# Optimization experiments

Measured on AMD Instinct MI355X. Metric: run time of the kernel, lower is better.

Reference implementation:

```python
import jax, jax.numpy as jnp
import numpy as np

EPS = 1e-5

def conv2d(x, w, b):
    # x: [B,C,H,W], w: [O,I,kh,kw], VALID padding, stride 1
    y = jax.lax.conv_general_dilated(x, w, (1, 1), 'VALID',
                                     dimension_numbers=('NCHW', 'OIHW', 'NCHW'))
    return y + b[None, :, None, None]

def batchnorm(x, g, b):
    # training-mode BN: batch statistics over (N,H,W), biased variance (torch semantics)
    m = jnp.mean(x, axis=(0, 2, 3), keepdims=True)
    v = jnp.mean((x - m) ** 2, axis=(0, 2, 3), keepdims=True)
    return g[None, :, None, None] * (x - m) / jnp.sqrt(v + EPS) + b[None, :, None, None]

def maxpool2(x):
    return jax.lax.reduce_window(x, -jnp.inf, jax.lax.max,
                                 (1, 1, 2, 2), (1, 1, 2, 2), 'VALID')

def self_attention(x, qw, qb, kw, kb, vw, vb, gamma):
    # x: [B,C,H,W]; qw/kw: [C//8, C]; vw: [C, C] (1x1 convs)
    B, C, H, W = x.shape
    xf = x.reshape(B, C, H * W)                               # [B,C,N]
    q = jnp.einsum('oc,bcn->bon', qw, xf) + qb[None, :, None]  # [B,C//8,N]
    k = jnp.einsum('oc,bcn->bon', kw, xf) + kb[None, :, None]
    v = jnp.einsum('oc,bcn->bon', vw, xf) + vb[None, :, None]  # [B,C,N]
    energy = jnp.einsum('bcn,bcm->bnm', q, k)                  # [B,N,N] (query n, key m)
    attn = jax.nn.softmax(energy, axis=-1)
    out = jnp.einsum('bcm,bnm->bcn', v, attn)                  # [B,C,N]
    return gamma * out.reshape(B, C, H, W) + x

def setup_inputs() -> dict:
    key = jax.random.key(0)
    ks = jax.random.split(key, 20)
    s = 0.05
    d = {}
    d['x'] = jax.random.normal(ks[0], (1, 3, 256, 256), jnp.float32)
    d['conv1_w'] = jax.random.normal(ks[1], (32, 3, 3, 3), jnp.float32) * s
    d['conv1_b'] = jnp.zeros((32,), jnp.float32)
    d['bn1_g'] = jnp.ones((32,), jnp.float32)
    d['bn1_b'] = jnp.zeros((32,), jnp.float32)
    d['a1_qw'] = jax.random.normal(ks[2], (4, 32), jnp.float32) * s
    d['a1_qb'] = jnp.zeros((4,), jnp.float32)
    d['a1_kw'] = jax.random.normal(ks[3], (4, 32), jnp.float32) * s
    d['a1_kb'] = jnp.zeros((4,), jnp.float32)
    d['a1_vw'] = jax.random.normal(ks[4], (32, 32), jnp.float32) * s
    d['a1_vb'] = jnp.zeros((32,), jnp.float32)
    d['a1_gamma'] = jnp.ones((1,), jnp.float32)
    d['conv2_w'] = jax.random.normal(ks[5], (64, 32, 3, 3), jnp.float32) * s
    d['conv2_b'] = jnp.zeros((64,), jnp.float32)
    d['bn2_g'] = jnp.ones((64,), jnp.float32)
    d['bn2_b'] = jnp.zeros((64,), jnp.float32)
    d['a2_qw'] = jax.random.normal(ks[6], (8, 64), jnp.float32) * s
    d['a2_qb'] = jnp.zeros((8,), jnp.float32)
    d['a2_kw'] = jax.random.normal(ks[7], (8, 64), jnp.float32) * s
    d['a2_kb'] = jnp.zeros((8,), jnp.float32)
    d['a2_vw'] = jax.random.normal(ks[8], (64, 64), jnp.float32) * s
    d['a2_vb'] = jnp.zeros((64,), jnp.float32)
    d['a2_gamma'] = jnp.ones((1,), jnp.float32)
    d['fc_w'] = jax.random.normal(ks[9], (50, 64 * 62 * 62), jnp.float32) * 0.002
    d['fc_b'] = jnp.zeros((50,), jnp.float32)
    return d

def reference(x, conv1_w, conv1_b, bn1_g, bn1_b,
              a1_qw, a1_qb, a1_kw, a1_kb, a1_vw, a1_vb, a1_gamma,
              conv2_w, conv2_b, bn2_g, bn2_b,
              a2_qw, a2_qb, a2_kw, a2_kb, a2_vw, a2_vb, a2_gamma,
              fc_w, fc_b):
    h = conv2d(x, conv1_w, conv1_b)                 # [B,32,254,254]
    h = jax.nn.relu(batchnorm(h, bn1_g, bn1_b))
    h = maxpool2(h)                                 # [B,32,127,127]
    h = self_attention(h, a1_qw, a1_qb, a1_kw, a1_kb, a1_vw, a1_vb, a1_gamma)
    h = conv2d(h, conv2_w, conv2_b)                 # [B,64,125,125]
    h = jax.nn.relu(batchnorm(h, bn2_g, bn2_b))
    h = maxpool2(h)                                 # [B,64,62,62]
    h = self_attention(h, a2_qw, a2_qb, a2_kw, a2_kb, a2_vw, a2_vb, a2_gamma)
    h = h.reshape(h.shape[0], -1)                   # [B, 64*62*62]
    return h @ fc_w.T + fc_b
```

## Files before the change

### kernel.cpp

```cpp
#include <hip/hip_runtime.h>
#include <hip/hip_bf16.h>

typedef float f32x4 __attribute__((ext_vector_type(4)));
typedef short bf16x8 __attribute__((ext_vector_type(8)));

__device__ inline unsigned short f2bf(float x) {
    __hip_bfloat16 h = __float2bfloat16(x);
    return *reinterpret_cast<unsigned short*>(&h);
}

template <int CIN, int ICB>
__launch_bounds__(256)
__global__ void conv3x3_rt_kernel(const float* __restrict__ src, int H, int W,
                                  const float* __restrict__ w,
                                  const float* __restrict__ b,
                                  float* __restrict__ dst, int OH, int OW,
                                  float* __restrict__ bn_accum) {
    __shared__ __align__(16) float xs[ICB][18][68];
    __shared__ __align__(16) float wsm[ICB][12];
    __shared__ float red[512];

    const int oc  = blockIdx.z;
    const int ox0 = blockIdx.x * 64;
    const int oy0 = blockIdx.y * 16;
    const int tid = threadIdx.x;
    const int ty  = tid >> 4;
    const int tx  = (tid & 15) << 2;

    float o0, o1, o2, o3;
    o0 = o1 = o2 = o3 = b[oc];

    const int scol   = tid & 63;
    const int sslot0 = tid >> 6;
    const bool colok = (ox0 + scol) < W;

    for (int icb = 0; icb < CIN; icb += ICB) {
        __syncthreads();
        {
            int s  = sslot0;
            int rr = sslot0;
            const float* gp = src + ((size_t)icb * H + oy0 + rr) * W + ox0 + scol;
            float* lp = &xs[0][0][0] + (size_t)s * 68 + scol;
            while (s < ICB * 18) {
                int y = oy0 + rr;
                *lp = (y < H && colok) ? *gp : 0.f;
                s += 4; rr += 4;
                gp += 4 * (size_t)W;
                lp += 4 * 68;
                if (rr >= 18) { rr -= 18; gp += ((size_t)H - 18) * W; }
            }
        }
        if (tid < ICB * 18) {
            int c = tid / 18, r = tid - c * 18;
            int y = oy0 + r;
            const float* gp = src + ((size_t)(icb + c) * H + y) * W + ox0 + 64;
            bool yok = (y < H);
            xs[c][r][64] = (yok && (ox0 + 64) < W) ? gp[0] : 0.f;
            xs[c][r][65] = (yok && (ox0 + 65) < W) ? gp[1] : 0.f;
        }
        if (tid < ICB * 9) {
            int c = tid / 9, j = tid - c * 9;
            wsm[c][j] = w[((size_t)oc * CIN + icb + c) * 9 + j];
        }
        __syncthreads();

        #pragma unroll
        for (int c = 0; c < ICB; ++c) {
            float wv[9];
            #pragma unroll
            for (int j = 0; j < 9; ++j) wv[j] = wsm[c][j];
            #pragma unroll
            for (int kh = 0; kh < 3; ++kh) {
                const float* xp = &xs[c][ty + kh][tx];
                f32x4 x03 = *(const f32x4*)xp;
                float x4 = xp[4], x5 = xp[5];
                const float w0 = wv[kh * 3], w1 = wv[kh * 3 + 1], w2 = wv[kh * 3 + 2];
                o0 = fmaf(x03[0], w0, o0); o0 = fmaf(x03[1], w1, o0); o0 = fmaf(x03[2], w2, o0);
                o1 = fmaf(x03[1], w0, o1); o1 = fmaf(x03[2], w1, o1); o1 = fmaf(x03[3], w2, o1);
                o2 = fmaf(x03[2], w0, o2); o2 = fmaf(x03[3], w1, o2); o2 = fmaf(x4,     w2, o2);
                o3 = fmaf(x03[3], w0, o3); o3 = fmaf(x4,     w1, o3); o3 = fmaf(x5,     w2, o3);
            }
        }
    }

    const int oy = oy0 + ty;
    const int ox = ox0 + tx;
    float s1 = 0.f, s2 = 0.f;
    if (oy < OH) {
        float* dp = dst + ((size_t)oc * OH + oy) * OW + ox;
        if (ox + 0 < OW) { dp[0] = o0; s1 += o0; s2 = fmaf(o0, o0, s2); }
        if (ox + 1 < OW) { dp[1] = o1; s1 += o1; s2 = fmaf(o1, o1, s2); }
        if (ox + 2 < OW) { dp[2] = o2; s1 += o2; s2 = fmaf(o2, o2, s2); }
        if (ox + 3 < OW) { dp[3] = o3; s1 += o3; s2 = fmaf(o3, o3, s2); }
    }
    red[tid]       = s1;
    red[256 + tid] = s2;
    __syncthreads();
    for (int off2 = 128; off2 > 0; off2 >>= 1) {
        if (tid < off2) {
            red[tid]       += red[tid + off2];
            red[256 + tid] += red[256 + tid + off2];
        }
        __syncthreads();
    }
    if (tid == 0) {
        atomicAdd(&bn_accum[oc * 2],     red[0]);
        atomicAdd(&bn_accum[oc * 2 + 1], red[256]);
    }
}

__global__ void bn_final_kernel(const float* __restrict__ sums, int C, int spatial,
                                const float* __restrict__ g, const float* __restrict__ bb,
                                float* __restrict__ inv_shift) {
    int c = threadIdx.x;
    if (c >= C) return;
    float m   = sums[c * 2] / (float)spatial;
    float var = sums[c * 2 + 1] / (float)spatial - m * m;
    float inv = g[c] * rsqrtf(var + 1e-5f);
    inv_shift[c * 2]     = inv;
    inv_shift[c * 2 + 1] = bb[c] - m * inv;
}

__global__ void bn_pool_kernel(const float* __restrict__ src,
                               const float* __restrict__ inv_shift,
                               int H, int W, int OH, int OW, int C,
                               float* __restrict__ dst) {
    int i = blockIdx.x * blockDim.x + threadIdx.x;
    if (i >= C * OH * OW) return;
    int ox = i % OW;
    int oy = (i / OW) % OH;
    int c  = i / (OW * OH);
    float inv = inv_shift[c * 2], sh = inv_shift[c * 2 + 1];
    const float* p = src + ((size_t)c * H + 2 * oy) * W + 2 * ox;
    float a = fmaxf(fmaf(p[0],     inv, sh), 0.f);
    float b = fmaxf(fmaf(p[1],     inv, sh), 0.f);
    float d = fmaxf(fmaf(p[W],     inv, sh), 0.f);
    float e = fmaxf(fmaf(p[W + 1], inv, sh), 0.f);
    dst[i] = fmaxf(fmaxf(a, b), fmaxf(d, e));
}

__global__ void qkv_proj_kernel(const float* __restrict__ xf, int N, int NP, int C, int Cqk,
                                const float* __restrict__ qw, const float* __restrict__ qb,
                                const float* __restrict__ kw, const float* __restrict__ kb,
                                const float* __restrict__ vw, const float* __restrict__ vb,
                                float* __restrict__ q, float* __restrict__ k,
                                unsigned short* __restrict__ v) {
    constexpr int OCG = 8;
    __shared__ float wl[OCG * 64 + OCG];
    const int g0 = blockIdx.y * OCG;
    const int tid = threadIdx.x;
    for (int i = tid; i < OCG * C; i += blockDim.x) {
        int o = i / C, cc = i % C;
        int oc = g0 + o;
        const float* wsrc = (oc < Cqk) ? (qw + oc * C)
                          : (oc < 2 * Cqk) ? (kw + (oc - Cqk) * C)
                          : (vw + (oc - 2 * Cqk) * C);
        wl[o * C + cc] = wsrc[cc];
    }
    if (tid < OCG) {
        int oc = g0 + tid;
        wl[OCG * C + tid] = (oc < Cqk) ? qb[oc]
                          : (oc < 2 * Cqk) ? kb[oc - Cqk]
                          : vb[oc - 2 * Cqk];
    }
    __syncthreads();
    int n = blockIdx.x * blockDim.x + tid;
    if (n >= N) return;
    float acc[OCG];
    #pragma unroll
    for (int o = 0; o < OCG; ++o) acc[o] = wl[OCG * C + o];
    for (int c = 0; c < C; ++c) {
        float xv = xf[(size_t)c * N + n];
        #pragma unroll
        for (int o = 0; o < OCG; ++o) acc[o] = fmaf(xv, wl[o * C + c], acc[o]);
    }
    #pragma unroll
    for (int o = 0; o < OCG; ++o) {
        int oc = g0 + o;
        if (oc < Cqk)            q[(size_t)oc * NP + n] = acc[o];
        else if (oc < 2 * Cqk)   k[(size_t)(oc - Cqk) * NP + n] = acc[o];
        else                     v[(size_t)(oc - 2 * Cqk) * NP + n] = f2bf(acc[o]);
    }
}

template <int CQK, int CV>
__launch_bounds__(256)
__global__ void flash_mfma_kernel(const float* __restrict__ q,
                                  const float* __restrict__ k,
                                  const unsigned short* __restrict__ v,
                                  int N, int NP, int chunk,
                                  float* __restrict__ l_part,
                                  float* __restrict__ acc_part) {
    constexpr int VS = 72;
    __shared__ float ksm[CQK * 64];
    __shared__ unsigned short vsm[CV * VS];
    const int tid  = threadIdx.x;
    const int wave = tid >> 6;
    const int lane = tid & 63;
    const int row  = lane & 15;
    const int g    = lane >> 4;
    const int s    = blockIdx.y;
    const int m0   = s * chunk;
    const int m1   = min(N, m0 + chunk);
    const int qb   = blockIdx.x * 64 + wave * 16;
    const int n    = qb + row;

    float qr[CQK];
    #pragma unroll
    for (int c = 0; c < CQK; ++c)
        qr[c] = (n < N) ? q[(size_t)c * NP + n] * 1.44269504f : 0.f;

    const int kc  = tid / 64,  kkk = tid % 64;
    const int vch = tid / 8,   vkk = (tid % 8) * 8;

    f32x4 acc[CV / 16];
    #pragma unroll
    for (int f = 0; f < CV / 16; ++f) acc[f] = (f32x4){0.f, 0.f, 0.f, 0.f};
    float lsum = 0.f;

    const int nchunks = (m1 - m0 + 63) >> 6;
    for (int t = 0; t < nchunks; ++t) {
        const int mt = m0 + t * 64;
        __syncthreads();
        #pragma unroll
        for (int cc = 0; cc < CQK / 4; ++cc)
            ksm[cc * 256 + tid] = k[(size_t)(kc + cc * 4) * NP + mt + kkk];
        #pragma unroll
        for (int vv = 0; vv < CV / 32; ++vv) {
            int ch = vch + vv * 32;
            ushort4 a0 = *(const ushort4*)&v[(size_t)ch * NP + mt + vkk];
            ushort4 a1 = *(const ushort4*)&v[(size_t)ch * NP + mt + vkk + 4];
            *(ushort4*)&vsm[ch * VS + vkk]     = a0;
            *(ushort4*)&vsm[ch * VS + vkk + 4] = a1;
        }
        __syncthreads();

        const bool tail = (mt + 64 > m1);
        #pragma unroll
        for (int h = 0; h < 2; ++h) {
            const int kk0 = h * 32 + 8 * g;
            f32x4 e0 = (f32x4){0.f, 0.f, 0.f, 0.f};
            f32x4 e1 = (f32x4){0.f, 0.f, 0.f, 0.f};
            #pragma unroll
            for (int c = 0; c < CQK; ++c) {
                f32x4 ka  = *(const f32x4*)&ksm[c * 64 + kk0];
                f32x4 kc2 = *(const f32x4*)&ksm[c * 64 + kk0 + 4];
                e0 += qr[c] * ka;
                e1 += qr[c] * kc2;
            }
            bf16x8 pfrag;
            if (!tail) {
                #pragma unroll
                for (int j = 0; j < 4; ++j) {
                    float p = exp2f(e0[j]); lsum += p; pfrag[j] = (short)f2bf(p);
                }
                #pragma unroll
                for (int j = 0; j < 4; ++j) {
                    float p = exp2f(e1[j]); lsum += p; pfrag[4 + j] = (short)f2bf(p);
                }
            } else {
                #pragma unroll
                for (int j = 0; j < 4; ++j) {
                    float p = (mt + kk0 + j < m1) ? exp2f(e0[j]) : 0.f;
                    lsum += p; pfrag[j] = (short)f2bf(p);
                }
                #pragma unroll
                for (int j = 0; j < 4; ++j) {
                    float p = (mt + kk0 + 4 + j < m1) ? exp2f(e1[j]) : 0.f;
                    lsum += p; pfrag[4 + j] = (short)f2bf(p);
                }
            }
            #pragma unroll
            for (int f = 0; f < CV / 16; ++f) {
                bf16x8 vf = *(const bf16x8*)&vsm[(f * 16 + row) * VS + kk0];
                acc[f] = __builtin_amdgcn_mfma_f32_16x16x32_bf16(pfrag, vf, acc[f], 0, 0, 0);
            }
        }
    }

    lsum += __shfl_xor(lsum, 16, 64);
    lsum += __shfl_xor(lsum, 32, 64);
    if (g == 0 && n < N) l_part[(size_t)s * N + n] = lsum;

    #pragma unroll
    for (int f = 0; f < CV / 16; ++f) {
        #pragma unroll
        for (int r2 = 0; r2 < 4; ++r2) {
            int nq = qb + 4 * g + r2;
            if (nq < N)
                acc_part[((size_t)s * N + nq) * CV + f * 16 + row] = acc[f][r2];
        }
    }
}

__global__ void combine_kernel(const float* __restrict__ acc_part,
                               const float* __restrict__ l_part,
                               int nsplit, int N, int CV,
                               const float* __restrict__ gamma,
                               const float* __restrict__ x_res,
                               float* __restrict__ out) {
    int n = blockIdx.x * blockDim.x + threadIdx.x;
    if (n >= N) return;
    int cv0 = blockIdx.y * 16;
    float l = 0.f;
    for (int s = 0; s < nsplit; ++s) l += l_part[(size_t)s * N + n];
    f32x4 a[4];
    #pragma unroll
    for (int t = 0; t < 4; ++t) a[t] = (f32x4){0.f, 0.f, 0.f, 0.f};
    for (int s = 0; s < nsplit; ++s) {
        const float* p = acc_part + ((size_t)s * N + n) * CV + cv0;
        #pragma unroll
        for (int t = 0; t < 4; ++t) a[t] += *(const f32x4*)(p + 4 * t);
    }
    float gs = gamma[0] / l;
    #pragma unroll
    for (int t = 0; t < 4; ++t)
        #pragma unroll
        for (int u = 0; u < 4; ++u) {
            int cv = cv0 + 4 * t + u;
            out[(size_t)cv * N + n] = fmaf(gs, a[t][u], x_res[(size_t)cv * N + n]);
        }
}

__global__ void fc_partial_kernel(const float* __restrict__ h, const float* __restrict__ w,
                                  int K, int nchunk, float* __restrict__ partial) {
    const int r = blockIdx.y, cb = blockIdx.x;
    const int chunk = K / nchunk;
    const int j0 = cb * chunk;
    const int j1 = (cb == nchunk - 1) ? K : j0 + chunk;
    const float* wr = w + (size_t)r * K;
    float s = 0.f;
    for (int j = j0 + (int)threadIdx.x * 4; j + 3 < j1; j += blockDim.x * 4) {
        float4 hv = *reinterpret_cast<const float4*>(h + j);
        float4 wv = *reinterpret_cast<const float4*>(wr + j);
        s += hv.x * wv.x + hv.y * wv.y + hv.z * wv.z + hv.w * wv.w;
    }
    __shared__ float red[256];
    red[threadIdx.x] = s;
    __syncthreads();
    for (int off = 128; off > 0; off >>= 1) {
        if ((int)threadIdx.x < off) red[threadIdx.x] += red[threadIdx.x + off];
        __syncthreads();
    }
    if (threadIdx.x == 0) partial[r * gridDim.x + cb] = red[0];
}

__global__ void fc_final_kernel(const float* __restrict__ partial,
                                const float* __restrict__ b, int nchunk,
                                float* __restrict__ out) {
    int r = threadIdx.x;
    if (r < 50) {
        float s = b[r];
        for (int i = 0; i < nchunk; ++i) s += partial[r * nchunk + i];
        out[r] = s;
    }
}

extern "C" void kernel_launch(void* const* d_in, const int* in_sizes, int n_in,
                              void* d_out, int out_size, void* d_ws, size_t ws_size,
                              hipStream_t stream) {
    const float* x    = (const float*)d_in[0];
    const float* c1w  = (const float*)d_in[1];
    const float* c1b  = (const float*)d_in[2];
    const float* bn1g = (const float*)d_in[3];
    const float* bn1b = (const float*)d_in[4];
    const float* a1qw = (const float*)d_in[5];
    const float* a1qb = (const float*)d_in[6];
    const float* a1kw = (const float*)d_in[7];
    const float* a1kb = (const float*)d_in[8];
    const float* a1vw = (const float*)d_in[9];
    const float* a1vb = (const float*)d_in[10];
    const float* a1g  = (const float*)d_in[11];
    const float* c2w  = (const float*)d_in[12];
    const float* c2b  = (const float*)d_in[13];
    const float* bn2g = (const float*)d_in[14];
    const float* bn2b = (const float*)d_in[15];
    const float* a2qw = (const float*)d_in[16];
    const float* a2qb = (const float*)d_in[17];
    const float* a2kw = (const float*)d_in[18];
    const float* a2kb = (const float*)d_in[19];
    const float* a2vw = (const float*)d_in[20];
    const float* a2vb = (const float*)d_in[21];
    const float* a2g  = (const float*)d_in[22];
    const float* fcw  = (const float*)d_in[23];
    const float* fcb  = (const float*)d_in[24];
    float* out = (float*)d_out;

    const int N1 = 127 * 127;
    const int N2 = 62 * 62;
    const int NP1 = (N1 + 63) & ~63;
    const int NP2 = (N2 + 63) & ~63;
    const int NS1 = 8, NS2 = 16;
    const int CH1 = 2048;
    const int CH2 = 256;

    char* base = (char*)d_ws;
    size_t off = 0;
    auto alloc = [&](size_t bytes) {
        void* p = base + off;
        off += (bytes + 63) & ~(size_t)63;
        return p;
    };
    float* h1     = (float*)alloc(sizeof(float) * 32 * 254 * 254);
    float* bnSums = (float*)alloc(sizeof(float) * 256);
    float* bnA    = (float*)alloc(sizeof(float) * 64);
    float* p1     = (float*)alloc(sizeof(float) * 32 * N1);
    float* q1     = (float*)alloc(sizeof(float) * 4 * NP1);
    float* k1     = (float*)alloc(sizeof(float) * 4 * NP1);
    unsigned short* v1 = (unsigned short*)alloc(sizeof(short) * 32 * NP1);
    float* l1     = (float*)alloc(sizeof(float) * NS1 * N1);
    float* a1p    = (float*)alloc(sizeof(float) * (size_t)NS1 * N1 * 32);
    float* ao1    = (float*)alloc(sizeof(float) * 32 * N1);
    float* h2     = (float*)alloc(sizeof(float) * 64 * 125 * 125);
    float* bnB    = (float*)alloc(sizeof(float) * 128);
    float* p2     = (float*)alloc(sizeof(float) * 64 * N2);
    float* q2     = (float*)alloc(sizeof(float) * 8 * NP2);
    float* k2     = (float*)alloc(sizeof(float) * 8 * NP2);
    unsigned short* v2 = (unsigned short*)alloc(sizeof(short) * 64 * NP2);
    float* l2     = (float*)alloc(sizeof(float) * NS2 * N2);
    float* a2p    = (float*)alloc(sizeof(float) * (size_t)NS2 * N2 * 64);
    float* ao2    = (float*)alloc(sizeof(float) * 64 * N2);
    float* fcp    = (float*)alloc(sizeof(float) * 2048);

    hipMemsetAsync(bnSums, 0, 256 * sizeof(float), stream);

    conv3x3_rt_kernel<3, 3><<<dim3(4, 16, 32), 256, 0, stream>>>(
        x, 256, 256, c1w, c1b, h1, 254, 254, bnSums);
    bn_final_kernel<<<1, 32, 0, stream>>>(bnSums, 32, 254 * 254, bn1g, bn1b, bnA);
    bn_pool_kernel<<<(32 * N1 + 255) / 256, 256, 0, stream>>>(
        h1, bnA, 254, 254, 127, 127, 32, p1);

    qkv_proj_kernel<<<dim3((N1 + 255) / 256, 5), 256, 0, stream>>>(
        p1, N1, NP1, 32, 4, a1qw, a1qb, a1kw, a1kb, a1vw, a1vb, q1, k1, v1);
    flash_mfma_kernel<4, 32><<<dim3((N1 + 63) / 64, NS1), 256, 0, stream>>>(
        q1, k1, v1, N1, NP1, CH1, l1, a1p);
    combine_kernel<<<dim3((N1 + 255) / 256, 2), 256, 0, stream>>>(
        a1p, l1, NS1, N1, 32, a1g, p1, ao1);

    conv3x3_rt_kernel<32, 8><<<dim3(2, 8, 64), 256, 0, stream>>>(
        ao1, 127, 127, c2w, c2b, h2, 125, 125, bnSums + 64);
    bn_final_kernel<<<1, 64, 0, stream>>>(bnSums + 64, 64, 125 * 125, bn2g, bn2b, bnB);
    bn_pool_kernel<<<(64 * N2 + 255) / 256, 256, 0, stream>>>(
        h2, bnB, 125, 125, 62, 62, 64, p2);

    qkv_proj_kernel<<<dim3((N2 + 255) / 256, 10), 256, 0, stream>>>(
        p2, N2, NP2, 64, 8, a2qw, a2qb, a2kw, a2kb, a2vw, a2vb, q2, k2, v2);
    flash_mfma_kernel<8, 64><<<dim3((N2 + 63) / 64, NS2), 256, 0, stream>>>(
        q2, k2, v2, N2, NP2, CH2, l2, a2p);
    combine_kernel<<<dim3((N2 + 255) / 256, 4), 256, 0, stream>>>(
        a2p, l2, NS2, N2, 64, a2g, p2, ao2);

    fc_partial_kernel<<<dim3(32, 50), 256, 0, stream>>>(ao2, fcw, 64 * N2, 32, fcp);
    fc_final_kernel<<<1, 64, 0, stream>>>(fcp, fcb, 32, out);
}
```

Baseline: 311.0 us.

## Compute QK energies with bf16 MFMA and double-buffer V tiles in flash attention

The projection kernel now writes Q (pre-scaled by log2e) and K as bf16 in a position-major layout. The flash kernel computes QK^T with 16x16x16 bf16 MFMA instead of scalar FMAs from shared K, and packs probabilities with v_cvt_pk_bf16. V tiles are prefetched into registers and double-buffered in LDS, so only one barrier is needed per tile. The first attention layer moves from 8 to 4 key splits with computed chunk sizes. Rounding Q and K to bf16 lowers the precision of the energies.

```diff
diff --git a/kernel.cpp b/kernel.cpp
--- a/kernel.cpp
+++ b/kernel.cpp
@@ -2,11 +2,19 @@
 #include <hip/hip_bf16.h>
 
 typedef float f32x4 __attribute__((ext_vector_type(4)));
-typedef short bf16x8 __attribute__((ext_vector_type(8)));
+typedef short bf16x4 __attribute__((ext_vector_type(4)));
+typedef unsigned short u16x4 __attribute__((ext_vector_type(4)));
+typedef unsigned short u16x8 __attribute__((ext_vector_type(8)));
 
 __device__ inline unsigned short f2bf(float x) {
     __hip_bfloat16 h = __float2bfloat16(x);
     return *reinterpret_cast<unsigned short*>(&h);
+}
+
+__device__ inline int cvt_pk_bf16(float a, float b) {
+    int r;
+    asm("v_cvt_pk_bf16_f32 %0, %1, %2" : "=v"(r) : "v"(a), "v"(b));
+    return r;
 }
 
 template <int CIN, int ICB>
@@ -143,8 +151,9 @@
                                 const float* __restrict__ qw, const float* __restrict__ qb,
                                 const float* __restrict__ kw, const float* __restrict__ kb,
                                 const float* __restrict__ vw, const float* __restrict__ vb,
-                                float* __restrict__ q, float* __restrict__ k,
-                                unsigned short* __restrict__ v) {
+                                unsigned short* __restrict__ qo,
+                                unsigned short* __restrict__ ko,
+                                unsigned short* __restrict__ vo) {
     constexpr int OCG = 8;
     __shared__ float wl[OCG * 64 + OCG];
     const int g0 = blockIdx.y * OCG;
@@ -174,108 +183,143 @@
         #pragma unroll
         for (int o = 0; o < OCG; ++o) acc[o] = fmaf(xv, wl[o * C + c], acc[o]);
     }
-    #pragma unroll
-    for (int o = 0; o < OCG; ++o) {
-        int oc = g0 + o;
-        if (oc < Cqk)            q[(size_t)oc * NP + n] = acc[o];
-        else if (oc < 2 * Cqk)   k[(size_t)(oc - Cqk) * NP + n] = acc[o];
-        else                     v[(size_t)(oc - 2 * Cqk) * NP + n] = f2bf(acc[o]);
+    const float LOG2E = 1.44269504f;
+    if (g0 < 2 * Cqk) {
+        if (Cqk == 4) {
+            u16x4 qs, ks;
+            #pragma unroll
+            for (int j = 0; j < 4; ++j) {
+                qs[j] = f2bf(acc[j] * LOG2E);
+                ks[j] = f2bf(acc[4 + j]);
+            }
+            *(u16x4*)&qo[(size_t)n * 4] = qs;
+            *(u16x4*)&ko[(size_t)n * 4] = ks;
+        } else {
+            unsigned short* dst = (g0 == 0) ? qo : ko;
+            float sc = (g0 == 0) ? LOG2E : 1.f;
+            u16x4 a, bb2;
+            #pragma unroll
+            for (int j = 0; j < 4; ++j) {
+                a[j]   = f2bf(acc[j] * sc);
+                bb2[j] = f2bf(acc[4 + j] * sc);
+            }
+            *(u16x4*)&dst[(size_t)n * 8]     = a;
+            *(u16x4*)&dst[(size_t)n * 8 + 4] = bb2;
+        }
+    } else {
+        #pragma unroll
+        for (int o = 0; o < OCG; ++o)
+            vo[(size_t)(g0 + o - 2 * Cqk) * NP + n] = f2bf(acc[o]);
     }
 }
 
 template <int CQK, int CV>
 __launch_bounds__(256)
-__global__ void flash_mfma_kernel(const float* __restrict__ q,
-                                  const float* __restrict__ k,
+__global__ void flash_mfma_kernel(const unsigned short* __restrict__ qbf,
+                                  const unsigned short* __restrict__ kbf,
                                   const unsigned short* __restrict__ v,
                                   int N, int NP, int chunk,
                                   float* __restrict__ l_part,
                                   float* __restrict__ acc_part) {
     constexpr int VS = 72;
-    __shared__ float ksm[CQK * 64];
-    __shared__ unsigned short vsm[CV * VS];
+    __shared__ unsigned short vsm[2][CV * VS];
     const int tid  = threadIdx.x;
     const int wave = tid >> 6;
     const int lane = tid & 63;
-    const int row  = lane & 15;
+    const int lq   = lane & 15;
     const int g    = lane >> 4;
     const int s    = blockIdx.y;
     const int m0   = s * chunk;
     const int m1   = min(N, m0 + chunk);
     const int qb   = blockIdx.x * 64 + wave * 16;
-    const int n    = qb + row;
-
-    float qr[CQK];
-    #pragma unroll
-    for (int c = 0; c < CQK; ++c)
-        qr[c] = (n < N) ? q[(size_t)c * NP + n] * 1.44269504f : 0.f;
-
-    const int kc  = tid / 64,  kkk = tid % 64;
-    const int vch = tid / 8,   vkk = (tid % 8) * 8;
+    const int n    = qb + lq;
+
+    bf16x4 qf = (bf16x4){0, 0, 0, 0};
+    if (g * 4 < CQK)
+        qf = *(const bf16x4*)&qbf[(size_t)n * CQK + 4 * g];
+
+    const int vch = tid >> 3;
+    const int vkk = (tid & 7) * 8;
 
     f32x4 acc[CV / 16];
     #pragma unroll
     for (int f = 0; f < CV / 16; ++f) acc[f] = (f32x4){0.f, 0.f, 0.f, 0.f};
     float lsum = 0.f;
 
-    const int nchunks = (m1 - m0 + 63) >> 6;
-    for (int t = 0; t < nchunks; ++t) {
-        const int mt = m0 + t * 64;
+    const int nch = (m1 - m0 + 63) >> 6;
+
+    u16x8 vreg[CV / 32];
+    #pragma unroll
+    for (int vv = 0; vv < CV / 32; ++vv)
+        vreg[vv] = *(const u16x8*)&v[(size_t)(vch + 32 * vv) * NP + m0 + vkk];
+    #pragma unroll
+    for (int vv = 0; vv < CV / 32; ++vv)
+        *(u16x8*)&vsm[0][(vch + 32 * vv) * VS + vkk] = vreg[vv];
+    __syncthreads();
+
+    for (int t = 0; t < nch; ++t) {
+        const int mt  = m0 + t * 64;
+        const int cur = t & 1;
+        const int mtn = (t + 1 < nch) ? mt + 64 : mt;
+        #pragma unroll
+        for (int vv = 0; vv < CV / 32; ++vv)
+            vreg[vv] = *(const u16x8*)&v[(size_t)(vch + 32 * vv) * NP + mtn + vkk];
+
+        bf16x4 kf[4];
+        #pragma unroll
+        for (int tt = 0; tt < 4; ++tt) {
+            kf[tt] = (bf16x4){0, 0, 0, 0};
+            if (g * 4 < CQK)
+                kf[tt] = *(const bf16x4*)&kbf[(size_t)(mt + 16 * tt + lq) * CQK + 4 * g];
+        }
+        f32x4 e[4];
+        #pragma unroll
+        for (int tt = 0; tt < 4; ++tt)
+            e[tt] = __builtin_amdgcn_mfma_f32_16x16x16bf16_1k(
+                kf[tt], qf, (f32x4){0.f, 0.f, 0.f, 0.f}, 0, 0, 0);
+
+        bf16x4 pf[4];
+        const bool tail = (mt + 64 > m1);
+        if (!tail) {
+            #pragma unroll
+            for (int tt = 0; tt < 4; ++tt) {
+                float p0 = exp2f(e[tt][0]), p1 = exp2f(e[tt][1]);
+                float p2 = exp2f(e[tt][2]), p3 = exp2f(e[tt][3]);
+                lsum += (p0 + p1) + (p2 + p3);
+                int2 pi;
+                pi.x = cvt_pk_bf16(p0, p1);
+                pi.y = cvt_pk_bf16(p2, p3);
+                pf[tt] = __builtin_bit_cast(bf16x4, pi);
+            }
+        } else {
+            #pragma unroll
+            for (int tt = 0; tt < 4; ++tt) {
+                int key = mt + 16 * tt + 4 * g;
+                float p0 = (key + 0 < m1) ? exp2f(e[tt][0]) : 0.f;
+                float p1 = (key + 1 < m1) ? exp2f(e[tt][1]) : 0.f;
+                float p2 = (key + 2 < m1) ? exp2f(e[tt][2]) : 0.f;
+                float p3 = (key + 3 < m1) ? exp2f(e[tt][3]) : 0.f;
+                lsum += (p0 + p1) + (p2 + p3);
+                int2 pi;
+                pi.x = cvt_pk_bf16(p0, p1);
+                pi.y = cvt_pk_bf16(p2, p3);
+                pf[tt] = __builtin_bit_cast(bf16x4, pi);
+            }
+        }
+
+        #pragma unroll
+        for (int tt = 0; tt < 4; ++tt) {
+            #pragma unroll
+            for (int f = 0; f < CV / 16; ++f) {
+                bf16x4 vf = *(const bf16x4*)&vsm[cur][(f * 16 + lq) * VS + 16 * tt + 4 * g];
+                acc[f] = __builtin_amdgcn_mfma_f32_16x16x16bf16_1k(pf[tt], vf, acc[f], 0, 0, 0);
+            }
+        }
+
+        #pragma unroll
+        for (int vv = 0; vv < CV / 32; ++vv)
+            *(u16x8*)&vsm[cur ^ 1][(vch + 32 * vv) * VS + vkk] = vreg[vv];
         __syncthreads();
-        #pragma unroll
-        for (int cc = 0; cc < CQK / 4; ++cc)
-            ksm[cc * 256 + tid] = k[(size_t)(kc + cc * 4) * NP + mt + kkk];
-        #pragma unroll
-        for (int vv = 0; vv < CV / 32; ++vv) {
-            int ch = vch + vv * 32;
-            ushort4 a0 = *(const ushort4*)&v[(size_t)ch * NP + mt + vkk];
-            ushort4 a1 = *(const ushort4*)&v[(size_t)ch * NP + mt + vkk + 4];
-            *(ushort4*)&vsm[ch * VS + vkk]     = a0;
-            *(ushort4*)&vsm[ch * VS + vkk + 4] = a1;
-        }
-        __syncthreads();
-
-        const bool tail = (mt + 64 > m1);
-        #pragma unroll
-        for (int h = 0; h < 2; ++h) {
-            const int kk0 = h * 32 + 8 * g;
-            f32x4 e0 = (f32x4){0.f, 0.f, 0.f, 0.f};
-            f32x4 e1 = (f32x4){0.f, 0.f, 0.f, 0.f};
-            #pragma unroll
-            for (int c = 0; c < CQK; ++c) {
-                f32x4 ka  = *(const f32x4*)&ksm[c * 64 + kk0];
-                f32x4 kc2 = *(const f32x4*)&ksm[c * 64 + kk0 + 4];
-                e0 += qr[c] * ka;
-                e1 += qr[c] * kc2;
-            }
-            bf16x8 pfrag;
-            if (!tail) {
-                #pragma unroll
-                for (int j = 0; j < 4; ++j) {
-                    float p = exp2f(e0[j]); lsum += p; pfrag[j] = (short)f2bf(p);
-                }
-                #pragma unroll
-                for (int j = 0; j < 4; ++j) {
-                    float p = exp2f(e1[j]); lsum += p; pfrag[4 + j] = (short)f2bf(p);
-                }
-            } else {
-                #pragma unroll
-                for (int j = 0; j < 4; ++j) {
-                    float p = (mt + kk0 + j < m1) ? exp2f(e0[j]) : 0.f;
-                    lsum += p; pfrag[j] = (short)f2bf(p);
-                }
-                #pragma unroll
-                for (int j = 0; j < 4; ++j) {
-                    float p = (mt + kk0 + 4 + j < m1) ? exp2f(e1[j]) : 0.f;
-                    lsum += p; pfrag[4 + j] = (short)f2bf(p);
-                }
-            }
-            #pragma unroll
-            for (int f = 0; f < CV / 16; ++f) {
-                bf16x8 vf = *(const bf16x8*)&vsm[(f * 16 + row) * VS + kk0];
-                acc[f] = __builtin_amdgcn_mfma_f32_16x16x32_bf16(pfrag, vf, acc[f], 0, 0, 0);
-            }
-        }
     }
 
     lsum += __shfl_xor(lsum, 16, 64);
@@ -288,7 +332,7 @@
         for (int r2 = 0; r2 < 4; ++r2) {
             int nq = qb + 4 * g + r2;
             if (nq < N)
-                acc_part[((size_t)s * N + nq) * CV + f * 16 + row] = acc[f][r2];
+                acc_part[((size_t)s * N + nq) * CV + f * 16 + lq] = acc[f][r2];
         }
     }
 }
@@ -390,9 +434,9 @@
     const int N2 = 62 * 62;
     const int NP1 = (N1 + 63) & ~63;
     const int NP2 = (N2 + 63) & ~63;
-    const int NS1 = 8, NS2 = 16;
-    const int CH1 = 2048;
-    const int CH2 = 256;
+    const int NS1 = 4, NS2 = 16;
+    const int CH1 = ((N1 + NS1 - 1) / NS1 + 63) & ~63;
+    const int CH2 = ((N2 + NS2 - 1) / NS2 + 63) & ~63;
 
     char* base = (char*)d_ws;
     size_t off = 0;
@@ -405,8 +449,8 @@
     float* bnSums = (float*)alloc(sizeof(float) * 256);
     float* bnA    = (float*)alloc(sizeof(float) * 64);
     float* p1     = (float*)alloc(sizeof(float) * 32 * N1);
-    float* q1     = (float*)alloc(sizeof(float) * 4 * NP1);
-    float* k1     = (float*)alloc(sizeof(float) * 4 * NP1);
+    unsigned short* q1 = (unsigned short*)alloc(sizeof(short) * NP1 * 4);
+    unsigned short* k1 = (unsigned short*)alloc(sizeof(short) * NP1 * 4);
     unsigned short* v1 = (unsigned short*)alloc(sizeof(short) * 32 * NP1);
     float* l1     = (float*)alloc(sizeof(float) * NS1 * N1);
     float* a1p    = (float*)alloc(sizeof(float) * (size_t)NS1 * N1 * 32);
@@ -414,8 +458,8 @@
     float* h2     = (float*)alloc(sizeof(float) * 64 * 125 * 125);
     float* bnB    = (float*)alloc(sizeof(float) * 128);
     float* p2     = (float*)alloc(sizeof(float) * 64 * N2);
-    float* q2     = (float*)alloc(sizeof(float) * 8 * NP2);
-    float* k2     = (float*)alloc(sizeof(float) * 8 * NP2);
+    unsigned short* q2 = (unsigned short*)alloc(sizeof(short) * NP2 * 8);
+    unsigned short* k2 = (unsigned short*)alloc(sizeof(short) * NP2 * 8);
     unsigned short* v2 = (unsigned short*)alloc(sizeof(short) * 64 * NP2);
     float* l2     = (float*)alloc(sizeof(float) * NS2 * N2);
     float* a2p    = (float*)alloc(sizeof(float) * (size_t)NS2 * N2 * 64);
```

Measured after the change: 297.9 us. -4.2%, faster.
